# Kernel optimization log

Measured on AMD Instinct MI355X. Metric: run time of the kernel, lower is better.

The kernel has to match this reference:

```python
import jax, jax.numpy as jnp
import numpy as np

B, S, HID, DEP, DS, NTYPES = 8, 128, 768, 64, 768, 45
NEG = -1000000000.0


def setup_inputs() -> dict:
    key = jax.random.key(0)
    ks = jax.random.split(key, 10)
    sc = lambda fan_in: 1.0 / np.sqrt(fan_in)
    return {
        "h": jax.random.normal(ks[0], (B, S, HID), dtype=jnp.float32),
        "dep_type_matrix": jax.random.randint(ks[1], (B, S, S), 0, NTYPES),
        "dep_emb_table": jax.random.normal(ks[2], (NTYPES, DEP), dtype=jnp.float32),
        # Linear weights stored as [in, out] so y = x @ W + b
        "W1_w": jax.random.normal(ks[3], (HID + DEP, DS), dtype=jnp.float32) * sc(HID + DEP),
        "W1_b": jnp.zeros((DS,), dtype=jnp.float32),
        "W2_w": jax.random.normal(ks[4], (HID + DEP, DS), dtype=jnp.float32) * sc(HID + DEP),
        "W2_b": jnp.zeros((DS,), dtype=jnp.float32),
        "gcn_w": jax.random.normal(ks[5], (HID, HID), dtype=jnp.float32) * sc(HID),
        "gcn_b": jnp.zeros((HID,), dtype=jnp.float32),
        "Wo_w": jax.random.normal(ks[6], (DS, HID), dtype=jnp.float32) * sc(DS),
        "Wo_b": jnp.zeros((HID,), dtype=jnp.float32),
    }


def reference(h, dep_type_matrix, dep_emb_table, W1_w, W1_b, W2_w, W2_b,
              gcn_w, gcn_b, Wo_w, Wo_b):
    adj = dep_type_matrix != 0                       # [B,S,S] bool
    dep_emb = dep_emb_table[dep_type_matrix]          # [B,S,S,DEP]

    # concat([h_i, dep_emb]) @ W1  ==  h_i @ W1[:HID] + dep_emb @ W1[HID:]
    hi_t = jnp.einsum('bid,de->bie', h, W1_w[:HID])[:, :, None, :] \
         + jnp.einsum('bijd,de->bije', dep_emb, W1_w[HID:]) + W1_b   # [B,S,S,DS]
    hj_t = jnp.einsum('bjd,de->bje', h, W2_w[:HID])[:, None, :, :] \
         + jnp.einsum('bijd,de->bije', dep_emb, W2_w[HID:]) + W2_b   # [B,S,S,DS]

    relevance = jnp.sum(hi_t * hj_t, axis=-1)         # [B,S,S]
    masked = jnp.where(adj, relevance, NEG)
    A = jax.nn.softmax(masked, axis=2)                # softmax over j

    h_syn = h
    for _ in range(1):  # num_layers = 1
        aggregated = jnp.einsum('bij,bjd->bid', A, h_syn)
        h_syn = jax.nn.relu(aggregated @ gcn_w + gcn_b)
    return h_syn @ Wo_w + Wo_b
```

## Files before the change

kernel.cpp:

```cpp
#include <hip/hip_runtime.h>
#include <hip/hip_bf16.h>

#define BB 8
#define SS 128
#define HID 768
#define DEP 64
#define DSZ 768
#define NT 45
#define NTP 48
#define NEG -1000000000.0f

typedef short bfv8 __attribute__((ext_vector_type(8)));
typedef float f32x4 __attribute__((ext_vector_type(4)));

__device__ __forceinline__ unsigned short f2bf(float x) {
    unsigned int u; __builtin_memcpy(&u, &x, 4);
    u += 0x7fffu + ((u >> 16) & 1u);
    return (unsigned short)(u >> 16);
}
__device__ __forceinline__ float bf2f(unsigned short h) {
    unsigned int u = ((unsigned int)h) << 16;
    float f; __builtin_memcpy(&f, &u, 4);
    return f;
}

__device__ __forceinline__ void gld16(const unsigned short* gp, unsigned short* lp) {
    typedef __attribute__((address_space(1))) const unsigned int GU;
    typedef __attribute__((address_space(3))) unsigned int LU;
    __builtin_amdgcn_global_load_lds((GU*)(uintptr_t)gp,
                                     (LU*)(unsigned int)(uintptr_t)lp, 16, 0, 0);
}

__global__ __launch_bounds__(256) void convec(
    const float* __restrict__ h, const float* __restrict__ table,
    const float* __restrict__ W1, const float* __restrict__ W2,
    const float* __restrict__ gcn, const float* __restrict__ Wo,
    unsigned short* __restrict__ hHi, unsigned short* __restrict__ hLo,
    unsigned short* __restrict__ WtHi, unsigned short* __restrict__ WtLo,
    unsigned short* __restrict__ gTHi, unsigned short* __restrict__ oTHi,
    unsigned short* __restrict__ Ehi, unsigned short* __restrict__ Elo,
    float* __restrict__ cv) {
    const long WN = (long)DSZ * HID;
    int tr = threadIdx.x >> 5, tc = threadIdx.x & 31;
    int z = blockIdx.z;
    if (z < 4) {
        __shared__ float tile[32][33];
        const float* src = z == 0 ? W1 : z == 1 ? W2 : z == 2 ? gcn : Wo;
        unsigned short* dhi = z == 0 ? WtHi : z == 1 ? WtHi + WN
                            : z == 2 ? gTHi : oTHi;
        unsigned short* dlo = z == 0 ? WtLo : z == 1 ? WtLo + WN : nullptr;
        int r0 = blockIdx.y * 32, c0 = blockIdx.x * 32;
#pragma unroll
        for (int k = 0; k < 4; ++k)
            tile[tr + k * 8][tc] = src[(long)(r0 + tr + k * 8) * 768 + c0 + tc];
        __syncthreads();
#pragma unroll
        for (int k = 0; k < 4; ++k) {
            int i = tr + k * 8, j = tc;
            float v = tile[j][i];
            unsigned short hh = f2bf(v);
            long o = (long)(c0 + i) * 768 + r0 + j;
            dhi[o] = hh;
            if (dlo) dlo[o] = f2bf(v - bf2f(hh));
        }
    } else if (z < 12) {
        if (blockIdx.y >= SS / 32) return;
        int b = z - 4;
        int r0 = blockIdx.y * 32, c0 = blockIdx.x * 32;
        const float* Xb = h + (long)b * SS * HID;
#pragma unroll
        for (int k = 0; k < 4; ++k) {
            int rr = r0 + tr + k * 8, cc = c0 + tc;
            float v = Xb[(long)rr * HID + cc];
            unsigned short hh = f2bf(v);
            long o = (long)b * SS * HID + (long)rr * HID + cc;
            hHi[o] = hh;
            hLo[o] = f2bf(v - bf2f(hh));
        }
    } else {
        if (blockIdx.y >= 2) return;
        int t = blockIdx.y * 24 + blockIdx.x;
        if (t >= NT) return;
        const long EN = (long)NTP * DSZ;
        __shared__ float tl[DEP];
        __shared__ float red[256];
        for (int d = threadIdx.x; d < DEP; d += 256) tl[d] = table[t * DEP + d];
        __syncthreads();
        float dotacc = 0.f;
#pragma unroll
        for (int k = 0; k < 3; ++k) {
            int e = threadIdx.x + k * 256;
            float s1 = 0.f, s2 = 0.f;
            for (int d = 0; d < DEP; ++d) {
                float td = tl[d];
                s1 += td * W1[(HID + d) * DSZ + e];
                s2 += td * W2[(HID + d) * DSZ + e];
            }
            long i0 = (long)t * DSZ + e;
            unsigned short h2 = f2bf(s2), h1 = f2bf(s1);
            Ehi[i0] = h2;      Elo[i0] = f2bf(s2 - bf2f(h2));
            Ehi[EN + i0] = h1; Elo[EN + i0] = f2bf(s1 - bf2f(h1));
            dotacc += s1 * s2;
        }
        red[threadIdx.x] = dotacc;
        __syncthreads();
        for (int w = 128; w >= 1; w >>= 1) {
            if (threadIdx.x < w) red[threadIdx.x] += red[threadIdx.x + w];
            __syncthreads();
        }
        if (threadIdx.x == 0) cv[t] = red[0];
    }
}

__global__ __launch_bounds__(256) void pgemm_direct(
    const unsigned short* __restrict__ hHi, const unsigned short* __restrict__ hLo,
    const unsigned short* __restrict__ WtHi, const unsigned short* __restrict__ WtLo,
    const float* __restrict__ b1, const float* __restrict__ b2,
    unsigned short* __restrict__ Phi, unsigned short* __restrict__ Plo) {
    const long MN = (long)BB * SS * DSZ;
    const long WN = (long)DSZ * HID;
    int which = blockIdx.z;
    int m0 = blockIdx.y * 128, n0 = blockIdx.x * 64;
    const unsigned short* bh = WtHi + (long)which * WN;
    const unsigned short* bl = WtLo + (long)which * WN;
    const float* bias = which ? b2 : b1;
    unsigned short* oh = Phi + (long)which * MN;
    unsigned short* ol = Plo + (long)which * MN;

    __shared__ __align__(16) unsigned short sAh[8192], sAl[8192];
    __shared__ __align__(16) unsigned short sBh[4096], sBl[4096];
    int tid = threadIdx.x, lane = tid & 63, wave = tid >> 6;
    int wr = wave >> 1, wc = wave & 1;
    int q = lane >> 4, r = lane & 15;

    f32x4 acc[4][2];
#pragma unroll
    for (int i = 0; i < 4; ++i)
#pragma unroll
        for (int j = 0; j < 2; ++j) acc[i][j] = (f32x4){0.f, 0.f, 0.f, 0.f};

    int arow0 = tid >> 2, ak0 = (tid & 3) << 3;
    int s1 = tid + 256;
    int arow1 = s1 >> 2, ak1 = (s1 & 3) << 3;
    const unsigned short* aP0 = hHi + (long)(m0 + arow0) * HID + ak0;
    const unsigned short* aP1 = hHi + (long)(m0 + arow1) * HID + ak1;
    const unsigned short* alP0 = hLo + (long)(m0 + arow0) * HID + ak0;
    const unsigned short* alP1 = hLo + (long)(m0 + arow1) * HID + ak1;
    const unsigned short* bP  = bh + (long)(n0 + arow0) * DSZ + ak0;
    const unsigned short* blP = bl + (long)(n0 + arow0) * DSZ + ak0;

    int aOff[4], bOff[2];
#pragma unroll
    for (int f = 0; f < 4; ++f) aOff[f] = (wr * 64 + f * 16 + r) * 32 + q * 8;
#pragma unroll
    for (int f = 0; f < 2; ++f) bOff[f] = (wc * 32 + f * 16 + r) * 32 + q * 8;

    auto stage = [&](int k0, int db) {
        unsigned short* a = sAh + db * 4096;
        unsigned short* al_ = sAl + db * 4096;
        unsigned short* b = sBh + db * 2048;
        unsigned short* bl_ = sBl + db * 2048;
        gld16(aP0 + k0, a + (wave << 9));
        gld16(aP1 + k0, a + 2048 + (wave << 9));
        gld16(alP0 + k0, al_ + (wave << 9));
        gld16(alP1 + k0, al_ + 2048 + (wave << 9));
        gld16(bP + k0, b + (wave << 9));
        gld16(blP + k0, bl_ + (wave << 9));
    };

    stage(0, 0);
    __syncthreads();
    int db = 0;
    for (int k0 = 0; k0 < HID; k0 += 32) {
        if (k0 + 32 < HID) stage(k0 + 32, db ^ 1);
        const unsigned short* cAh = sAh + db * 4096;
        const unsigned short* cAl = sAl + db * 4096;
        const unsigned short* cBh = sBh + db * 2048;
        const unsigned short* cBl = sBl + db * 2048;
        bfv8 b0h = *(const bfv8*)(cBh + bOff[0]);
        bfv8 b1h = *(const bfv8*)(cBh + bOff[1]);
        bfv8 b0l = *(const bfv8*)(cBl + bOff[0]);
        bfv8 b1l = *(const bfv8*)(cBl + bOff[1]);
#pragma unroll
        for (int fr = 0; fr < 4; ++fr) {
            bfv8 a_h = *(const bfv8*)(cAh + aOff[fr]);
            bfv8 a_l = *(const bfv8*)(cAl + aOff[fr]);
            acc[fr][0] = __builtin_amdgcn_mfma_f32_16x16x32_bf16(a_h, b0h, acc[fr][0], 0, 0, 0);
            acc[fr][0] = __builtin_amdgcn_mfma_f32_16x16x32_bf16(a_h, b0l, acc[fr][0], 0, 0, 0);
            acc[fr][0] = __builtin_amdgcn_mfma_f32_16x16x32_bf16(a_l, b0h, acc[fr][0], 0, 0, 0);
            acc[fr][1] = __builtin_amdgcn_mfma_f32_16x16x32_bf16(a_h, b1h, acc[fr][1], 0, 0, 0);
            acc[fr][1] = __builtin_amdgcn_mfma_f32_16x16x32_bf16(a_h, b1l, acc[fr][1], 0, 0, 0);
            acc[fr][1] = __builtin_amdgcn_mfma_f32_16x16x32_bf16(a_l, b1h, acc[fr][1], 0, 0, 0);
        }
        __syncthreads();
        db ^= 1;
    }
#pragma unroll
    for (int fr = 0; fr < 4; ++fr) {
        int rr = m0 + wr * 64 + fr * 16 + q * 4;
#pragma unroll
        for (int fc = 0; fc < 2; ++fc) {
            int cc = n0 + wc * 32 + fc * 16 + r;
            float bv = bias[cc];
#pragma unroll
            for (int i = 0; i < 4; ++i) {
                float v = acc[fr][fc][i] + bv;
                unsigned short hh = f2bf(v);
                long o = (long)(rr + i) * DSZ + cc;
                oh[o] = hh;
                ol[o] = f2bf(v - bf2f(hh));
            }
        }
    }
}

__device__ __forceinline__ void mfma_core(
    const unsigned short* __restrict__ ah, const unsigned short* __restrict__ al,
    const unsigned short* __restrict__ bh, const unsigned short* __restrict__ bl,
    float* __restrict__ Cb, int K, int kb, int kend, int ldc, int Nvalid,
    int m0, int n0, unsigned short* smem) {
    unsigned short* sAh = smem;
    unsigned short* sAl = smem + 8192;
    unsigned short* sBh = smem + 16384;
    unsigned short* sBl = smem + 24576;
    int tid = threadIdx.x;
    int lane = tid & 63, wave = tid >> 6;
    int wr = wave >> 1, wc = wave & 1;
    int q = lane >> 4, r = lane & 15;

    f32x4 acc[4][4];
#pragma unroll
    for (int i = 0; i < 4; ++i)
#pragma unroll
        for (int j = 0; j < 4; ++j) acc[i][j] = (f32x4){0.f, 0.f, 0.f, 0.f};

    int s0 = tid, s1 = tid + 256;
    int arow0 = s0 >> 2, ak0 = (s0 & 3) << 3;
    int arow1 = s1 >> 2, ak1 = (s1 & 3) << 3;
    const unsigned short* aP0 = ah + (long)(m0 + arow0) * K + ak0;
    const unsigned short* aP1 = ah + (long)(m0 + arow1) * K + ak1;
    bool bok0 = (n0 + arow0) < Nvalid, bok1 = (n0 + arow1) < Nvalid;
    const unsigned short* bP0 = bh + (long)(n0 + arow0) * K + ak0;
    const unsigned short* bP1 = bh + (long)(n0 + arow1) * K + ak1;
    const unsigned short* alP0 = al + (long)(m0 + arow0) * K + ak0;
    const unsigned short* alP1 = al + (long)(m0 + arow1) * K + ak1;
    const unsigned short* blP0 = bl + (long)(n0 + arow0) * K + ak0;
    const unsigned short* blP1 = bl + (long)(n0 + arow1) * K + ak1;

    int aOff[4], bOff[4];
#pragma unroll
    for (int f = 0; f < 4; ++f) {
        aOff[f] = (wr * 64 + f * 16 + r) * 32 + q * 8;
        bOff[f] = (wc * 64 + f * 16 + r) * 32 + q * 8;
    }

    auto stage = [&](int k0, int db) {
        unsigned short* a = sAh + db * 4096;
        unsigned short* al_ = sAl + db * 4096;
        unsigned short* b = sBh + db * 4096;
        unsigned short* bl_ = sBl + db * 4096;
        gld16(aP0 + k0, a + (wave << 9));
        gld16(aP1 + k0, a + 2048 + (wave << 9));
        gld16(alP0 + k0, al_ + (wave << 9));
        gld16(alP1 + k0, al_ + 2048 + (wave << 9));
        if (bok0) gld16(bP0 + k0, b + (wave << 9));
        if (bok1) gld16(bP1 + k0, b + 2048 + (wave << 9));
        if (bok0) gld16(blP0 + k0, bl_ + (wave << 9));
        if (bok1) gld16(blP1 + k0, bl_ + 2048 + (wave << 9));
    };

    stage(kb, 0);
    __syncthreads();
    int db = 0;
    for (int k0 = kb; k0 < kend; k0 += 32) {
        if (k0 + 32 < kend) stage(k0 + 32, db ^ 1);
        const unsigned short* cAh = sAh + db * 4096;
        const unsigned short* cAl = sAl + db * 4096;
        const unsigned short* cBh = sBh + db * 4096;
        const unsigned short* cBl = sBl + db * 4096;
        bfv8 bh_r[4], bl_r[4];
#pragma unroll
        for (int fc = 0; fc < 4; ++fc) {
            bh_r[fc] = *(const bfv8*)(cBh + bOff[fc]);
            bl_r[fc] = *(const bfv8*)(cBl + bOff[fc]);
        }
#pragma unroll
        for (int fr = 0; fr < 4; ++fr) {
            bfv8 a_h = *(const bfv8*)(cAh + aOff[fr]);
            bfv8 a_l = *(const bfv8*)(cAl + aOff[fr]);
#pragma unroll
            for (int fc = 0; fc < 4; ++fc) {
                acc[fr][fc] = __builtin_amdgcn_mfma_f32_16x16x32_bf16(a_h, bh_r[fc], acc[fr][fc], 0, 0, 0);
                acc[fr][fc] = __builtin_amdgcn_mfma_f32_16x16x32_bf16(a_h, bl_r[fc], acc[fr][fc], 0, 0, 0);
                acc[fr][fc] = __builtin_amdgcn_mfma_f32_16x16x32_bf16(a_l, bh_r[fc], acc[fr][fc], 0, 0, 0);
            }
        }
        __syncthreads();
        db ^= 1;
    }
#pragma unroll
    for (int fr = 0; fr < 4; ++fr) {
        int rr = m0 + wr * 64 + fr * 16 + q * 4;
#pragma unroll
        for (int fc = 0; fc < 4; ++fc) {
            int cc = n0 + wc * 64 + fc * 16 + r;
            if (cc < Nvalid) {
#pragma unroll
                for (int i = 0; i < 4; ++i)
                    Cb[(long)(rr + i) * ldc + cc] = acc[fr][fc][i];
            }
        }
    }
}

__global__ __launch_bounds__(256) void uvgram_hg(
    const unsigned short* __restrict__ Phi, const unsigned short* __restrict__ Plo,
    const unsigned short* __restrict__ EtHi, const unsigned short* __restrict__ EtLo,
    float* __restrict__ UVP, float* __restrict__ GP,
    const unsigned short* __restrict__ hHi, const unsigned short* __restrict__ gTHi,
    unsigned short* __restrict__ HGT) {
    const long MN = (long)BB * SS * DSZ;
    const long EN = (long)NTP * DSZ;
    const long UVN = (long)BB * SS * NTP;
    const long BSD = (long)SS * DSZ;
    __shared__ __align__(16) unsigned short smem[32768];
    int id = blockIdx.x;
    if (id < 64) {
        int y = id >> 3, z = id & 7;
        int which = z >> 2, split = z & 3;
        mfma_core(Phi + (long)which * MN, Plo + (long)which * MN,
                  EtHi + (long)which * EN, EtLo + (long)which * EN,
                  UVP + (long)which * 4 * UVN + (long)split * UVN,
                  DSZ, split * 192, split * 192 + 192, NTP, NTP,
                  y * 128, 0, smem);
    } else if (id < 128) {
        int g = id - 64;
        int b = g >> 3, split = g & 7;
        mfma_core(Phi + (long)b * BSD, Plo + (long)b * BSD,
                  Phi + MN + (long)b * BSD, Plo + MN + (long)b * BSD,
                  GP + (long)b * 8 * (SS * SS) + (long)split * (SS * SS),
                  DSZ, split * 96, split * 96 + 96, SS, SS,
                  0, 0, smem);
    } else {
        int hgid = id - 128;
        int n0 = (hgid % 12) * 64, m0 = (hgid / 12) * 64;
        unsigned short* sA = smem;
        unsigned short* sB = smem + 4096;
        int tid = threadIdx.x, lane = tid & 63, wave = tid >> 6;
        int wr = wave >> 1, wc = wave & 1;
        int q = lane >> 4, r = lane & 15;
        f32x4 acc[2][2];
#pragma unroll
        for (int i = 0; i < 2; ++i)
#pragma unroll
            for (int j = 0; j < 2; ++j) acc[i][j] = (f32x4){0.f, 0.f, 0.f, 0.f};
        int arow = tid >> 2, ak = (tid & 3) << 3;
        const unsigned short* aP = hHi + (long)(m0 + arow) * HID + ak;
        const unsigned short* bP = gTHi + (long)(n0 + arow) * HID + ak;
        int aOff[2], bOff[2];
#pragma unroll
        for (int f = 0; f < 2; ++f) {
            aOff[f] = (wr * 32 + f * 16 + r) * 32 + q * 8;
            bOff[f] = (wc * 32 + f * 16 + r) * 32 + q * 8;
        }
        auto stage = [&](int k0, int db) {
            gld16(aP + k0, sA + db * 2048 + (wave << 9));
            gld16(bP + k0, sB + db * 2048 + (wave << 9));
        };
        stage(0, 0);
        __syncthreads();
        int db = 0;
        for (int k0 = 0; k0 < HID; k0 += 32) {
            if (k0 + 32 < HID) stage(k0 + 32, db ^ 1);
            const unsigned short* cA = sA + db * 2048;
            const unsigned short* cB = sB + db * 2048;
            bfv8 b0 = *(const bfv8*)(cB + bOff[0]);
            bfv8 b1 = *(const bfv8*)(cB + bOff[1]);
#pragma unroll
            for (int fr = 0; fr < 2; ++fr) {
                bfv8 a = *(const bfv8*)(cA + aOff[fr]);
                acc[fr][0] = __builtin_amdgcn_mfma_f32_16x16x32_bf16(a, b0, acc[fr][0], 0, 0, 0);
                acc[fr][1] = __builtin_amdgcn_mfma_f32_16x16x32_bf16(a, b1, acc[fr][1], 0, 0, 0);
            }
            __syncthreads();
            db ^= 1;
        }
#pragma unroll
        for (int fr = 0; fr < 2; ++fr) {
            int rr = m0 + wr * 32 + fr * 16 + q * 4;
#pragma unroll
            for (int fc = 0; fc < 2; ++fc) {
                int cc = n0 + wc * 32 + fc * 16 + r;
#pragma unroll
                for (int i = 0; i < 4; ++i) {
                    int m = rr + i;
                    long o = (long)(m >> 7) * ((long)HID * SS) + (long)cc * SS + (m & 127);
                    HGT[o] = f2bf(acc[fr][fc][i]);
                }
            }
        }
    }
}

template <int OUT>
__global__ __launch_bounds__(256) void gemm64(
    const unsigned short* __restrict__ Ahi, const unsigned short* __restrict__ Bhi,
    const float* __restrict__ bias, unsigned short* __restrict__ Chi,
    float* __restrict__ Cf, int relu, int K, int ldc,
    long sA, long sB, long sC) {
    int batch = blockIdx.z;
    int m0 = blockIdx.y * 64, n0 = blockIdx.x * 64;
    const unsigned short* ah = Ahi + (long)batch * sA;
    const unsigned short* bh = Bhi + (long)batch * sB;

    __shared__ __align__(16) unsigned short sAh[4096], sBh[4096];
    int tid = threadIdx.x;
    int lane = tid & 63, wave = tid >> 6;
    int wr = wave >> 1, wc = wave & 1;
    int q = lane >> 4, r = lane & 15;

    f32x4 acc[2][2];
#pragma unroll
    for (int i = 0; i < 2; ++i)
#pragma unroll
        for (int j = 0; j < 2; ++j) acc[i][j] = (f32x4){0.f, 0.f, 0.f, 0.f};

    int arow = tid >> 2, ak = (tid & 3) << 3;
    const unsigned short* aP = ah + (long)(m0 + arow) * K + ak;
    const unsigned short* bP = bh + (long)(n0 + arow) * K + ak;

    int aOff[2], bOff[2];
#pragma unroll
    for (int f = 0; f < 2; ++f) {
        aOff[f] = (wr * 32 + f * 16 + r) * 32 + q * 8;
        bOff[f] = (wc * 32 + f * 16 + r) * 32 + q * 8;
    }

    auto stage = [&](int k0, int db) {
        gld16(aP + k0, sAh + db * 2048 + (wave << 9));
        gld16(bP + k0, sBh + db * 2048 + (wave << 9));
    };
    stage(0, 0);
    __syncthreads();
    int db = 0;
    for (int k0 = 0; k0 < K; k0 += 32) {
        if (k0 + 32 < K) stage(k0 + 32, db ^ 1);
        const unsigned short* cA = sAh + db * 2048;
        const unsigned short* cB = sBh + db * 2048;
        bfv8 b0 = *(const bfv8*)(cB + bOff[0]);
        bfv8 b1 = *(const bfv8*)(cB + bOff[1]);
#pragma unroll
        for (int fr = 0; fr < 2; ++fr) {
            bfv8 a = *(const bfv8*)(cA + aOff[fr]);
            acc[fr][0] = __builtin_amdgcn_mfma_f32_16x16x32_bf16(a, b0, acc[fr][0], 0, 0, 0);
            acc[fr][1] = __builtin_amdgcn_mfma_f32_16x16x32_bf16(a, b1, acc[fr][1], 0, 0, 0);
        }
        __syncthreads();
        db ^= 1;
    }
#pragma unroll
    for (int fr = 0; fr < 2; ++fr) {
        int rr = m0 + wr * 32 + fr * 16 + q * 4;
#pragma unroll
        for (int fc = 0; fc < 2; ++fc) {
            int cc = n0 + wc * 32 + fc * 16 + r;
            float bv = bias ? bias[cc] : 0.f;
#pragma unroll
            for (int i = 0; i < 4; ++i) {
                float v = acc[fr][fc][i] + bv;
                if constexpr (OUT == 1) {
                    if (relu) v = fmaxf(v, 0.f);
                    Chi[(long)batch * sC + (long)(rr + i) * ldc + cc] = f2bf(v);
                } else {
                    Cf[(long)batch * sC + (long)(rr + i) * ldc + cc] = v;
                }
            }
        }
    }
}

__global__ __launch_bounds__(128) void softmax_kernel(
    const int* __restrict__ dep, const float* __restrict__ Gp,
    const float* __restrict__ Up, const float* __restrict__ cv,
    unsigned short* __restrict__ Ahi) {
    const long UVN = (long)BB * SS * NTP;
    int bi = blockIdx.x;
    int b = bi >> 7;
    int j = threadIdx.x;
    int t = dep[(long)bi * SS + j];
    float r;
    if (t != 0) {
        long gbase = (long)bi * SS + j + (long)b * 7L * SS * SS;
        float g = 0.f;
        for (int s = 0; s < 8; ++s) g += Gp[gbase + (long)s * (SS * SS)];
        float su = 0.f, sv = 0.f;
        long ui = (long)bi * NTP + t;
        long vi = ((long)b * SS + j) * NTP + t;
        for (int s = 0; s < 4; ++s) {
            su += Up[(long)s * UVN + ui];
            sv += Up[(long)(4 + s) * UVN + vi];
        }
        r = g + su + sv + cv[t];
    } else {
        r = NEG;
    }
    float m = r;
    for (int off = 1; off < 64; off <<= 1) m = fmaxf(m, __shfl_xor(m, off));
    __shared__ float smax[2], ssum[2];
    if ((threadIdx.x & 63) == 0) smax[threadIdx.x >> 6] = m;
    __syncthreads();
    m = fmaxf(smax[0], smax[1]);
    float p = expf(r - m);
    float s = p;
    for (int off = 1; off < 64; off <<= 1) s += __shfl_xor(s, off);
    if ((threadIdx.x & 63) == 0) ssum[threadIdx.x >> 6] = s;
    __syncthreads();
    s = ssum[0] + ssum[1];
    Ahi[(long)bi * SS + j] = f2bf(p / s);
}

__global__ void e_kernel(const float* __restrict__ table,
                         const float* __restrict__ W1,
                         const float* __restrict__ W2,
                         float* __restrict__ Ef) {
    int idx = blockIdx.x * blockDim.x + threadIdx.x;
    if (idx >= NTP * DSZ) return;
    int t = idx / DSZ, e = idx % DSZ;
    float s1 = 0.f, s2 = 0.f;
    if (t < NT)
        for (int d = 0; d < DEP; ++d) {
            float td = table[t * DEP + d];
            s1 += td * W1[(HID + d) * DSZ + e];
            s2 += td * W2[(HID + d) * DSZ + e];
        }
    const long EN = (long)NTP * DSZ;
    Ef[idx] = s2; Ef[EN + idx] = s1;
}

__global__ void c_kernel(const float* __restrict__ Ef, float* __restrict__ cv) {
    int t = blockIdx.x;
    const long EN = (long)NTP * DSZ;
    float s = 0.f;
    for (int e = threadIdx.x; e < DSZ; e += 256)
        s += Ef[(long)t * DSZ + e] * Ef[EN + (long)t * DSZ + e];
    __shared__ float red[256];
    red[threadIdx.x] = s;
    __syncthreads();
    for (int w = 128; w >= 1; w >>= 1) {
        if (threadIdx.x < w) red[threadIdx.x] += red[threadIdx.x + w];
        __syncthreads();
    }
    if (threadIdx.x == 0) cv[t] = red[0];
}

__device__ __forceinline__ void gemm_body(
    const float* __restrict__ Ab, const float* __restrict__ Bb,
    const float* __restrict__ bias, float* __restrict__ Cb,
    int kbeg, int kend, int lda, int ldb, int ldc,
    int row0, int col0, bool relu) {
    __shared__ float As[16][68];
    __shared__ float Bs[16][68];
    int tx = threadIdx.x & 15, ty = threadIdx.x >> 4;
    float acc[4][4] = {};
    for (int k0 = kbeg; k0 < kend; k0 += 16) {
#pragma unroll
        for (int l = 0; l < 4; ++l) {
            int idx = threadIdx.x + l * 256;
            int r = idx >> 4, kk = idx & 15;
            As[kk][r] = Ab[(long)(row0 + r) * lda + k0 + kk];
            int kk2 = idx >> 6, cc = idx & 63;
            Bs[kk2][cc] = Bb[(long)(k0 + kk2) * ldb + col0 + cc];
        }
        __syncthreads();
#pragma unroll
        for (int kk = 0; kk < 16; ++kk) {
            float4 a4 = *(const float4*)&As[kk][ty * 4];
            float4 b4 = *(const float4*)&Bs[kk][tx * 4];
            float a[4] = {a4.x, a4.y, a4.z, a4.w};
            float b[4] = {b4.x, b4.y, b4.z, b4.w};
#pragma unroll
            for (int i = 0; i < 4; ++i)
#pragma unroll
                for (int j = 0; j < 4; ++j) acc[i][j] += a[i] * b[j];
        }
        __syncthreads();
    }
#pragma unroll
    for (int i = 0; i < 4; ++i) {
        int r = row0 + ty * 4 + i;
#pragma unroll
        for (int j = 0; j < 4; ++j) {
            int c = col0 + tx * 4 + j;
            float v = acc[i][j];
            if (bias) v += bias[c];
            if (relu) v = fmaxf(v, 0.f);
            Cb[(long)r * ldc + c] = v;
        }
    }
}

__global__ __launch_bounds__(256) void gemm_k(
    const float* __restrict__ A, const float* __restrict__ B,
    const float* __restrict__ bias, float* __restrict__ C,
    int K, int nsplit, int lda, int ldb, int ldc,
    long sA, long sB, long sC, long splitStride, int relu) {
    int batch = blockIdx.z / nsplit, split = blockIdx.z % nsplit;
    int kc = K / nsplit;
    const float* Ab = A + (long)batch * sA;
    const float* Bb = B + (long)batch * sB;
    float* Cb = C + (long)batch * sC + (long)split * splitStride;
    gemm_body(Ab, Bb, nsplit == 1 ? bias : nullptr, Cb,
              split * kc, split * kc + kc, lda, ldb, ldc,
              blockIdx.y * 64, blockIdx.x * 64, relu && nsplit == 1);
}

__global__ __launch_bounds__(256) void gram32(
    const float* __restrict__ P1, const float* __restrict__ P2,
    float* __restrict__ Gp) {
    int b = blockIdx.z;
    int i0 = blockIdx.y * 32, j0 = blockIdx.x * 32;
    __shared__ float As[32][33];
    __shared__ float Bs[32][33];
    const float* p1 = P1 + (long)b * SS * DSZ;
    const float* p2 = P2 + (long)b * SS * DSZ;
    int tx = threadIdx.x % 32, ty = threadIdx.x / 32;
    float acc[4] = {0.f, 0.f, 0.f, 0.f};
    for (int k0 = 0; k0 < DSZ; k0 += 32) {
#pragma unroll
        for (int l = 0; l < 4; ++l) {
            int idx = threadIdx.x + l * 256;
            int r = idx / 32, kk = idx % 32;
            As[kk][r] = p1[(long)(i0 + r) * DSZ + k0 + kk];
            Bs[kk][r] = p2[(long)(j0 + r) * DSZ + k0 + kk];
        }
        __syncthreads();
#pragma unroll
        for (int kk = 0; kk < 32; ++kk) {
            float bv = Bs[kk][tx];
#pragma unroll
            for (int i = 0; i < 4; ++i) acc[i] += As[kk][ty * 4 + i] * bv;
        }
        __syncthreads();
    }
#pragma unroll
    for (int i = 0; i < 4; ++i)
        Gp[((long)b * SS + i0 + ty * 4 + i) * SS + j0 + tx] = acc[i];
}

__global__ __launch_bounds__(256) void uv_kernel(
    const float* __restrict__ P1, const float* __restrict__ P2,
    const float* __restrict__ E1, const float* __restrict__ E2,
    const float* __restrict__ cv, float* __restrict__ U, float* __restrict__ V) {
    int bs = blockIdx.x;
    __shared__ float p1[DSZ], p2[DSZ];
    for (int e = threadIdx.x; e < DSZ; e += 256) {
        p1[e] = P1[(long)bs * DSZ + e];
        p2[e] = P2[(long)bs * DSZ + e];
    }
    __syncthreads();
    int wave = threadIdx.x / 64, lane = threadIdx.x % 64;
    for (int t = wave; t < NT; t += 4) {
        float su = 0.f, sv = 0.f;
        for (int e = lane; e < DSZ; e += 64) {
            su += p1[e] * E2[(long)t * DSZ + e];
            sv += p2[e] * E1[(long)t * DSZ + e];
        }
        for (int off = 32; off >= 1; off >>= 1) {
            su += __shfl_down(su, off);
            sv += __shfl_down(sv, off);
        }
        if (lane == 0) {
            U[(long)bs * NTP + t] = su;
            V[(long)bs * NTP + t] = sv + cv[t];
        }
    }
}

__global__ __launch_bounds__(128) void softmax_fb(
    const int* __restrict__ dep, const float* __restrict__ G,
    const float* __restrict__ U, const float* __restrict__ V,
    float* __restrict__ A) {
    int bi = blockIdx.x;
    int b = bi >> 7;
    int j = threadIdx.x;
    int t = dep[(long)bi * SS + j];
    float r;
    if (t != 0)
        r = G[(long)bi * SS + j] + U[(long)bi * NTP + t] + V[((long)b * SS + j) * NTP + t];
    else
        r = NEG;
    float m = r;
    for (int off = 1; off < 64; off <<= 1) m = fmaxf(m, __shfl_xor(m, off));
    __shared__ float smax[2], ssum[2];
    if ((threadIdx.x & 63) == 0) smax[threadIdx.x >> 6] = m;
    __syncthreads();
    m = fmaxf(smax[0], smax[1]);
    float p = expf(r - m);
    float s = p;
    for (int off = 1; off < 64; off <<= 1) s += __shfl_xor(s, off);
    if ((threadIdx.x & 63) == 0) ssum[threadIdx.x >> 6] = s;
    __syncthreads();
    s = ssum[0] + ssum[1];
    A[(long)bi * SS + j] = p / s;
}

extern "C" void kernel_launch(void* const* d_in, const int* in_sizes, int n_in,
                              void* d_out, int out_size, void* d_ws, size_t ws_size,
                              hipStream_t stream) {
    const float* h      = (const float*)d_in[0];
    const int*   dep    = (const int*)d_in[1];
    const float* table  = (const float*)d_in[2];
    const float* W1_w   = (const float*)d_in[3];
    const float* W1_b   = (const float*)d_in[4];
    const float* W2_w   = (const float*)d_in[5];
    const float* W2_b   = (const float*)d_in[6];
    const float* gcn_w  = (const float*)d_in[7];
    const float* gcn_b  = (const float*)d_in[8];
    const float* Wo_w   = (const float*)d_in[9];
    const float* Wo_b   = (const float*)d_in[10];
    float* out = (float*)d_out;

    const long nBS = (long)BB * SS;
    const long MN  = nBS * DSZ;
    const long BSS = (long)BB * SS * SS;
    const long UVN = nBS * NTP;
    const long EN  = (long)NTP * DSZ;
    const long WN  = (long)DSZ * HID;
    const long BSD = (long)SS * DSZ;

    char* base = (char*)d_ws;
    size_t off = 0;
    auto alloc = [&](size_t bytes) -> void* {
        void* p = base + off;
        off += (bytes + 255) & ~(size_t)255;
        return p;
    };

    float* CV    = (float*)alloc(256);
    float* GP    = (float*)alloc(8 * BSS * 4);
    float* UVP   = (float*)alloc(8 * UVN * 4);
    unsigned short* EtHi = (unsigned short*)alloc(2 * EN * 2);
    unsigned short* EtLo = (unsigned short*)alloc(2 * EN * 2);
    unsigned short* hHi  = (unsigned short*)alloc(MN * 2);
    unsigned short* hLo  = (unsigned short*)alloc(MN * 2);
    unsigned short* WtHi = (unsigned short*)alloc(2 * WN * 2);
    unsigned short* WtLo = (unsigned short*)alloc(2 * WN * 2);
    unsigned short* gTHi = (unsigned short*)alloc(WN * 2);
    unsigned short* oTHi = (unsigned short*)alloc(WN * 2);
    unsigned short* Phi  = (unsigned short*)alloc(2 * MN * 2);
    unsigned short* Plo  = (unsigned short*)alloc(2 * MN * 2);
    unsigned short* AmHi = (unsigned short*)alloc(BSS * 2);
    unsigned short* HGT  = (unsigned short*)alloc(MN * 2);
    unsigned short* HSHi = (unsigned short*)alloc(MN * 2);
    size_t needBig = off;

    if (ws_size >= needBig) {
        convec<<<dim3(24, 24, 13), 256, 0, stream>>>(
            h, table, W1_w, W2_w, gcn_w, Wo_w,
            hHi, hLo, WtHi, WtLo, gTHi, oTHi, EtHi, EtLo, CV);
        pgemm_direct<<<dim3(12, 8, 2), 256, 0, stream>>>(
            hHi, hLo, WtHi, WtLo, W1_b, W2_b, Phi, Plo);
        uvgram_hg<<<320, 256, 0, stream>>>(
            Phi, Plo, EtHi, EtLo, UVP, GP, hHi, gTHi, HGT);
        softmax_kernel<<<nBS, 128, 0, stream>>>(dep, GP, UVP, CV, AmHi);
        gemm64<1><<<dim3(12, 2, 8), 256, 0, stream>>>(
            AmHi, HGT, gcn_b, HSHi, nullptr, 1, SS, HID,
            (long)SS * SS, (long)HID * SS, BSD);
        gemm64<2><<<dim3(12, 16, 1), 256, 0, stream>>>(
            HSHi, oTHi, Wo_b, nullptr, out, 0, DSZ, HID, 0, 0, 0);
    } else {
        float* ws = (float*)d_ws;
        long o2 = 0;
        float* Ef2  = ws + o2; o2 += 2 * EN;
        float* CV2  = ws + o2; o2 += 64;
        float* P1   = ws + o2; o2 += MN;
        float* P2   = ws + o2; o2 += MN;
        float* Uf   = ws + o2; o2 += UVN;
        float* Vf   = ws + o2; o2 += UVN;
        float* G    = ws + o2; o2 += BSS;
        float* Amat = ws + o2; o2 += BSS;
        float* AGG  = ws + o2; o2 += MN;
        float* HSYN = ws + o2; o2 += MN;

        e_kernel<<<(NTP * DSZ + 255) / 256, 256, 0, stream>>>(table, W1_w, W2_w, Ef2);
        c_kernel<<<NT, 256, 0, stream>>>(Ef2, CV2);
        gemm_k<<<dim3(DSZ / 64, nBS / 64, 1), 256, 0, stream>>>(
            h, W1_w, W1_b, P1, HID, 1, HID, DSZ, DSZ, 0, 0, 0, 0, 0);
        gemm_k<<<dim3(DSZ / 64, nBS / 64, 1), 256, 0, stream>>>(
            h, W2_w, W2_b, P2, HID, 1, HID, DSZ, DSZ, 0, 0, 0, 0, 0);
        uv_kernel<<<nBS, 256, 0, stream>>>(P1, P2, Ef2 + EN, Ef2, CV2, Uf, Vf);
        gram32<<<dim3(SS / 32, SS / 32, BB), 256, 0, stream>>>(P1, P2, G);
        softmax_fb<<<nBS, 128, 0, stream>>>(dep, G, Uf, Vf, Amat);
        gemm_k<<<dim3(HID / 64, SS / 64, BB), 256, 0, stream>>>(
            Amat, h, nullptr, AGG, SS, 1, SS, HID, HID,
            (long)SS * SS, BSD, BSD, 0, 0);
        gemm_k<<<dim3(HID / 64, nBS / 64, 1), 256, 0, stream>>>(
            AGG, gcn_w, gcn_b, HSYN, HID, 1, HID, HID, HID, 0, 0, 0, 0, 1);
        gemm_k<<<dim3(HID / 64, nBS / 64, 1), 256, 0, stream>>>(
            HSYN, Wo_w, Wo_b, out, DSZ, 1, DSZ, HID, HID, 0, 0, 0, 0, 0);
    }
}
```

Measured before the change: 74.80 us.

## Move h@gcn_w GEMM blocks from uvgram launch into projection GEMM launch

Moves the independent h·gcn_w (HGT) tile work out of the uvgram kernel and into the projection GEMM launch, giving a combined 384-block kernel. uvgram now launches only its 128 UV/Gram blocks. The intent is to fill idle CUs during the 192-block projection GEMM with the 192 HG tiles, and to shorten the uvgram launch, which was otherwise a tail of small blocks. The projection blocks now share a single 48KB shared buffer, and the larger combined kernel may leave a load imbalance between the heavy and light block types.

```diff
diff --git a/kernel.cpp b/kernel.cpp
--- a/kernel.cpp
+++ b/kernel.cpp
@@ -112,23 +112,24 @@
     }
 }
 
-__global__ __launch_bounds__(256) void pgemm_direct(
+__device__ __forceinline__ void pgemm_body(
     const unsigned short* __restrict__ hHi, const unsigned short* __restrict__ hLo,
     const unsigned short* __restrict__ WtHi, const unsigned short* __restrict__ WtLo,
     const float* __restrict__ b1, const float* __restrict__ b2,
-    unsigned short* __restrict__ Phi, unsigned short* __restrict__ Plo) {
+    unsigned short* __restrict__ Phi, unsigned short* __restrict__ Plo,
+    int which, int m0, int n0, unsigned short* smem) {
     const long MN = (long)BB * SS * DSZ;
     const long WN = (long)DSZ * HID;
-    int which = blockIdx.z;
-    int m0 = blockIdx.y * 128, n0 = blockIdx.x * 64;
     const unsigned short* bh = WtHi + (long)which * WN;
     const unsigned short* bl = WtLo + (long)which * WN;
     const float* bias = which ? b2 : b1;
     unsigned short* oh = Phi + (long)which * MN;
     unsigned short* ol = Plo + (long)which * MN;
 
-    __shared__ __align__(16) unsigned short sAh[8192], sAl[8192];
-    __shared__ __align__(16) unsigned short sBh[4096], sBl[4096];
+    unsigned short* sAh = smem;
+    unsigned short* sAl = smem + 8192;
+    unsigned short* sBh = smem + 16384;
+    unsigned short* sBl = smem + 20480;
     int tid = threadIdx.x, lane = tid & 63, wave = tid >> 6;
     int wr = wave >> 1, wc = wave & 1;
     int q = lane >> 4, r = lane & 15;
@@ -211,6 +212,84 @@
                 ol[o] = f2bf(v - bf2f(hh));
             }
         }
+    }
+}
+
+__device__ __forceinline__ void hg_body(
+    const unsigned short* __restrict__ hHi, const unsigned short* __restrict__ gTHi,
+    unsigned short* __restrict__ HGT, int m0, int n0, unsigned short* smem) {
+    unsigned short* sA = smem;
+    unsigned short* sB = smem + 4096;
+    int tid = threadIdx.x, lane = tid & 63, wave = tid >> 6;
+    int wr = wave >> 1, wc = wave & 1;
+    int q = lane >> 4, r = lane & 15;
+    f32x4 acc[2][2];
+#pragma unroll
+    for (int i = 0; i < 2; ++i)
+#pragma unroll
+        for (int j = 0; j < 2; ++j) acc[i][j] = (f32x4){0.f, 0.f, 0.f, 0.f};
+    int arow = tid >> 2, ak = (tid & 3) << 3;
+    const unsigned short* aP = hHi + (long)(m0 + arow) * HID + ak;
+    const unsigned short* bP = gTHi + (long)(n0 + arow) * HID + ak;
+    int aOff[2], bOff[2];
+#pragma unroll
+    for (int f = 0; f < 2; ++f) {
+        aOff[f] = (wr * 32 + f * 16 + r) * 32 + q * 8;
+        bOff[f] = (wc * 32 + f * 16 + r) * 32 + q * 8;
+    }
+    auto stage = [&](int k0, int db) {
+        gld16(aP + k0, sA + db * 2048 + (wave << 9));
+        gld16(bP + k0, sB + db * 2048 + (wave << 9));
+    };
+    stage(0, 0);
+    __syncthreads();
+    int db = 0;
+    for (int k0 = 0; k0 < HID; k0 += 32) {
+        if (k0 + 32 < HID) stage(k0 + 32, db ^ 1);
+        const unsigned short* cA = sA + db * 2048;
+        const unsigned short* cB = sB + db * 2048;
+        bfv8 b0 = *(const bfv8*)(cB + bOff[0]);
+        bfv8 b1 = *(const bfv8*)(cB + bOff[1]);
+#pragma unroll
+        for (int fr = 0; fr < 2; ++fr) {
+            bfv8 a = *(const bfv8*)(cA + aOff[fr]);
+            acc[fr][0] = __builtin_amdgcn_mfma_f32_16x16x32_bf16(a, b0, acc[fr][0], 0, 0, 0);
+            acc[fr][1] = __builtin_amdgcn_mfma_f32_16x16x32_bf16(a, b1, acc[fr][1], 0, 0, 0);
+        }
+        __syncthreads();
+        db ^= 1;
+    }
+#pragma unroll
+    for (int fr = 0; fr < 2; ++fr) {
+        int rr = m0 + wr * 32 + fr * 16 + q * 4;
+#pragma unroll
+        for (int fc = 0; fc < 2; ++fc) {
+            int cc = n0 + wc * 32 + fc * 16 + r;
+#pragma unroll
+            for (int i = 0; i < 4; ++i) {
+                int m = rr + i;
+                long o = (long)(m >> 7) * ((long)HID * SS) + (long)cc * SS + (m & 127);
+                HGT[o] = f2bf(acc[fr][fc][i]);
+            }
+        }
+    }
+}
+
+__global__ __launch_bounds__(256) void pgemm_hg(
+    const unsigned short* __restrict__ hHi, const unsigned short* __restrict__ hLo,
+    const unsigned short* __restrict__ WtHi, const unsigned short* __restrict__ WtLo,
+    const float* __restrict__ b1, const float* __restrict__ b2,
+    unsigned short* __restrict__ Phi, unsigned short* __restrict__ Plo,
+    const unsigned short* __restrict__ gTHi, unsigned short* __restrict__ HGT) {
+    __shared__ __align__(16) unsigned short smem[24576];
+    int id = blockIdx.x;
+    if (id < 192) {
+        int which = id / 96, v = id % 96;
+        pgemm_body(hHi, hLo, WtHi, WtLo, b1, b2, Phi, Plo,
+                   which, (v / 12) * 128, (v % 12) * 64, smem);
+    } else {
+        int hgid = id - 192;
+        hg_body(hHi, gTHi, HGT, (hgid / 12) * 64, (hgid % 12) * 64, smem);
     }
 }
 
@@ -313,12 +392,10 @@
     }
 }
 
-__global__ __launch_bounds__(256) void uvgram_hg(
+__global__ __launch_bounds__(256) void uvgram(
     const unsigned short* __restrict__ Phi, const unsigned short* __restrict__ Plo,
     const unsigned short* __restrict__ EtHi, const unsigned short* __restrict__ EtLo,
-    float* __restrict__ UVP, float* __restrict__ GP,
-    const unsigned short* __restrict__ hHi, const unsigned short* __restrict__ gTHi,
-    unsigned short* __restrict__ HGT) {
+    float* __restrict__ UVP, float* __restrict__ GP) {
     const long MN = (long)BB * SS * DSZ;
     const long EN = (long)NTP * DSZ;
     const long UVN = (long)BB * SS * NTP;
@@ -333,7 +410,7 @@
                   UVP + (long)which * 4 * UVN + (long)split * UVN,
                   DSZ, split * 192, split * 192 + 192, NTP, NTP,
                   y * 128, 0, smem);
-    } else if (id < 128) {
+    } else {
         int g = id - 64;
         int b = g >> 3, split = g & 7;
         mfma_core(Phi + (long)b * BSD, Plo + (long)b * BSD,
@@ -341,64 +418,6 @@
                   GP + (long)b * 8 * (SS * SS) + (long)split * (SS * SS),
                   DSZ, split * 96, split * 96 + 96, SS, SS,
                   0, 0, smem);
-    } else {
-        int hgid = id - 128;
-        int n0 = (hgid % 12) * 64, m0 = (hgid / 12) * 64;
-        unsigned short* sA = smem;
-        unsigned short* sB = smem + 4096;
-        int tid = threadIdx.x, lane = tid & 63, wave = tid >> 6;
-        int wr = wave >> 1, wc = wave & 1;
-        int q = lane >> 4, r = lane & 15;
-        f32x4 acc[2][2];
-#pragma unroll
-        for (int i = 0; i < 2; ++i)
-#pragma unroll
-            for (int j = 0; j < 2; ++j) acc[i][j] = (f32x4){0.f, 0.f, 0.f, 0.f};
-        int arow = tid >> 2, ak = (tid & 3) << 3;
-        const unsigned short* aP = hHi + (long)(m0 + arow) * HID + ak;
-        const unsigned short* bP = gTHi + (long)(n0 + arow) * HID + ak;
-        int aOff[2], bOff[2];
-#pragma unroll
-        for (int f = 0; f < 2; ++f) {
-            aOff[f] = (wr * 32 + f * 16 + r) * 32 + q * 8;
-            bOff[f] = (wc * 32 + f * 16 + r) * 32 + q * 8;
-        }
-        auto stage = [&](int k0, int db) {
-            gld16(aP + k0, sA + db * 2048 + (wave << 9));
-            gld16(bP + k0, sB + db * 2048 + (wave << 9));
-        };
-        stage(0, 0);
-        __syncthreads();
-        int db = 0;
-        for (int k0 = 0; k0 < HID; k0 += 32) {
-            if (k0 + 32 < HID) stage(k0 + 32, db ^ 1);
-            const unsigned short* cA = sA + db * 2048;
-            const unsigned short* cB = sB + db * 2048;
-            bfv8 b0 = *(const bfv8*)(cB + bOff[0]);
-            bfv8 b1 = *(const bfv8*)(cB + bOff[1]);
-#pragma unroll
-            for (int fr = 0; fr < 2; ++fr) {
-                bfv8 a = *(const bfv8*)(cA + aOff[fr]);
-                acc[fr][0] = __builtin_amdgcn_mfma_f32_16x16x32_bf16(a, b0, acc[fr][0], 0, 0, 0);
-                acc[fr][1] = __builtin_amdgcn_mfma_f32_16x16x32_bf16(a, b1, acc[fr][1], 0, 0, 0);
-            }
-            __syncthreads();
-            db ^= 1;
-        }
-#pragma unroll
-        for (int fr = 0; fr < 2; ++fr) {
-            int rr = m0 + wr * 32 + fr * 16 + q * 4;
-#pragma unroll
-            for (int fc = 0; fc < 2; ++fc) {
-                int cc = n0 + wc * 32 + fc * 16 + r;
-#pragma unroll
-                for (int i = 0; i < 4; ++i) {
-                    int m = rr + i;
-                    long o = (long)(m >> 7) * ((long)HID * SS) + (long)cc * SS + (m & 127);
-                    HGT[o] = f2bf(acc[fr][fc][i]);
-                }
-            }
-        }
     }
 }
 
@@ -758,10 +777,9 @@
         convec<<<dim3(24, 24, 13), 256, 0, stream>>>(
             h, table, W1_w, W2_w, gcn_w, Wo_w,
             hHi, hLo, WtHi, WtLo, gTHi, oTHi, EtHi, EtLo, CV);
-        pgemm_direct<<<dim3(12, 8, 2), 256, 0, stream>>>(
-            hHi, hLo, WtHi, WtLo, W1_b, W2_b, Phi, Plo);
-        uvgram_hg<<<320, 256, 0, stream>>>(
-            Phi, Plo, EtHi, EtLo, UVP, GP, hHi, gTHi, HGT);
+        pgemm_hg<<<384, 256, 0, stream>>>(
+            hHi, hLo, WtHi, WtLo, W1_b, W2_b, Phi, Plo, gTHi, HGT);
+        uvgram<<<128, 256, 0, stream>>>(Phi, Plo, EtHi, EtLo, UVP, GP);
         softmax_kernel<<<nBS, 128, 0, stream>>>(dep, GP, UVP, CV, AmHi);
         gemm64<1><<<dim3(12, 2, 8), 256, 0, stream>>>(
             AmHi, HGT, gcn_b, HSHi, nullptr, 1, SS, HID,
```

After: 71.04 us (median of 2 runs). 1.05x faster.
